# Kernel tuning notes

Hardware: AMD Instinct MI355X
Metric: run time of the kernel (lower is better)

Reference implementation:

```python
import jax, jax.numpy as jnp
import numpy as np

MAX_ITERATIONS = 10
TOLERANCE = 1e-4


def setup_inputs() -> dict:
    key = jax.random.key(0)
    k1, k2 = jax.random.split(key)
    B, N = 4, 2048
    p1 = jax.random.normal(k1, (B, N, 3), dtype=jnp.float32)
    p2 = jax.random.normal(k2, (B, N, 3), dtype=jnp.float32)
    return {"p1": p1, "p2": p2}


def _get_transform(p1, p2):
    # SVD-based rigid (Kabsch) transform between matched sets p1 -> p2.
    p1c = p1.mean(-2, keepdims=True)   # [B,1,3]
    p2c = p2.mean(-2, keepdims=True)   # [B,1,3]
    q1 = p1 - p1c
    q2 = p2 - p2c
    H = jnp.einsum('bnj,bnk->bjk', q2, q1)          # p2^T @ p1, [B,3,3]
    u, s, vT = jnp.linalg.svd(H)
    v = jnp.swapaxes(vT, -1, -2)
    uT = jnp.swapaxes(u, -1, -2)
    d = jnp.linalg.det(v @ uT)                      # [B], reflection fix
    v = v.at[:, 2, 2].multiply(d)
    RT = u @ jnp.swapaxes(v, -1, -2)
    R = jnp.swapaxes(RT, -1, -2)                    # [B,3,3]
    t = p2c - p1c @ R                               # [B,1,3]
    return R, t


def _nearest_neighbor(p1, p2):
    # dist[b, j, i] = ||p2[b,j] - p1[b,i]||  (matches torch broadcast layout)
    dif = p2[:, :, None, :] - p1[:, None, :, :]     # [B,N2,N1,3]
    dist = jnp.sqrt(jnp.sum(dif * dif, axis=-1))    # [B,N2,N1]
    idx = jnp.argmin(dist, axis=-1)                 # [B,N2] (topk k=1, smallest)
    vals = jnp.take_along_axis(dist, idx[..., None], axis=-1)[..., 0]
    return vals, idx


def reference(p1, p2):
    def cond(state):
        temp_pc, it, prev_err, done = state
        return (it <= MAX_ITERATIONS) & jnp.logical_not(done)

    def body(state):
        temp_pc, it, prev_err, _ = state
        vals, idx = _nearest_neighbor(temp_pc, p2)
        mean_err = vals.mean()
        # Source indexes ori_p2 with the LAST batch's indices (nn.indices[-1])
        matched = p2[:, idx[-1], :]                 # [B,N,3]
        R, t = _get_transform(temp_pc, matched)
        new_pc = temp_pc @ R + t
        done = jnp.abs(prev_err - mean_err) < TOLERANCE
        return (new_pc, it + 1, mean_err, done)

    init = (p1, jnp.int32(0), jnp.float32(0.0), jnp.bool_(False))
    temp_pc, _, _, _ = jax.lax.while_loop(cond, body, init)

    R, t = _get_transform(p1, temp_pc)
    T = jnp.concatenate([R, jnp.swapaxes(t, 1, 2)], axis=2)  # [B,3,4]
    return T
```

## Files before the change

kernel.cpp:

```cpp
#include <hip/hip_runtime.h>

#define B 4
#define N 2048
#define MAXIT 11
#define TOL 1e-4f
#define BT 256
#define NBLK 256
#define CC 64
#define QPT 4
#define QC (BT*QPT)
#define RPT 8


__device__ double det3(const double* M) {
    return M[0]*(M[4]*M[8]-M[5]*M[7])
         - M[1]*(M[3]*M[8]-M[5]*M[6])
         + M[2]*(M[3]*M[7]-M[4]*M[6]);
}

__device__ void svd3x3(const double* A, double* U, double* V, double* sig) {
    double S[9];
    for (int i = 0; i < 3; ++i)
        for (int j = 0; j < 3; ++j) {
            double s = 0.0;
            for (int k = 0; k < 3; ++k) s += A[k*3+i] * A[k*3+j];
            S[i*3+j] = s;
        }
    double Vm[9] = {1,0,0, 0,1,0, 0,0,1};
    for (int sweep = 0; sweep < 30; ++sweep) {
        double off = fabs(S[1]) + fabs(S[2]) + fabs(S[5]);
        double base = fabs(S[0]) + fabs(S[4]) + fabs(S[8]);
        if (off <= 1e-15 * base) break;
        for (int pi = 0; pi < 3; ++pi) {
            const int p = (pi == 2) ? 1 : 0;
            const int q = (pi == 0) ? 1 : 2;
            double apq = S[p*3+q];
            if (apq == 0.0) continue;
            double app = S[p*3+p], aqq = S[q*3+q];
            double tau = (aqq - app) / (2.0 * apq);
            double tt  = ((tau >= 0.0) ? 1.0 : -1.0) / (fabs(tau) + sqrt(1.0 + tau*tau));
            double c = 1.0 / sqrt(1.0 + tt*tt);
            double s = tt * c;
            for (int k = 0; k < 3; ++k) {
                double skp = S[k*3+p], skq = S[k*3+q];
                S[k*3+p] = c*skp - s*skq;
                S[k*3+q] = s*skp + c*skq;
            }
            for (int k = 0; k < 3; ++k) {
                double spk = S[p*3+k], sqk = S[q*3+k];
                S[p*3+k] = c*spk - s*sqk;
                S[q*3+k] = s*spk + c*sqk;
            }
            for (int k = 0; k < 3; ++k) {
                double vkp = Vm[k*3+p], vkq = Vm[k*3+q];
                Vm[k*3+p] = c*vkp - s*vkq;
                Vm[k*3+q] = s*vkp + c*vkq;
            }
        }
    }
    double lam[3] = {S[0], S[4], S[8]};
    int ord[3] = {0, 1, 2};
    for (int i = 0; i < 2; ++i)
        for (int j = i+1; j < 3; ++j)
            if (lam[ord[j]] > lam[ord[i]]) { int tmp = ord[i]; ord[i] = ord[j]; ord[j] = tmp; }
    for (int i = 0; i < 3; ++i) {
        int o = ord[i];
        double l = lam[o] > 0.0 ? lam[o] : 0.0;
        sig[i] = sqrt(l);
        for (int k = 0; k < 3; ++k) V[k*3+i] = Vm[k*3+o];
    }
    for (int i = 0; i < 3; ++i) {
        double u0 = 0, u1 = 0, u2 = 0;
        for (int k = 0; k < 3; ++k) {
            u0 += A[0*3+k] * V[k*3+i];
            u1 += A[1*3+k] * V[k*3+i];
            u2 += A[2*3+k] * V[k*3+i];
        }
        double nrm = sqrt(u0*u0 + u1*u1 + u2*u2);
        if (nrm > 1e-300) { u0 /= nrm; u1 /= nrm; u2 /= nrm; }
        else {
            double ax = U[0], ay = U[3], az = U[6];
            double bx = U[1], by = U[4], bz = U[7];
            u0 = ay*bz - az*by; u1 = az*bx - ax*bz; u2 = ax*by - ay*bx;
        }
        U[0*3+i] = u0; U[1*3+i] = u1; U[2*3+i] = u2;
    }
}

__device__ void compute_R_f64(const double* H, double* R) {
    double nf = 0.0;
    for (int k = 0; k < 9; ++k) nf += H[k]*H[k];
    if (nf > 0.0) {
        const double sc = 1.0 / sqrt(nf * (1.0/3.0));
        double X[9];
        #pragma unroll
        for (int k = 0; k < 9; ++k) X[k] = H[k] * sc;
        const double d0 = det3(X);
        if (d0 > 1e-12) {
            for (int iter = 0; iter < 10; ++iter) {
                const double dt = det3(X);
                const double g = (iter < 4) ? cbrt(1.0 / dt) : 1.0;
                double Y[9];
                #pragma unroll
                for (int k = 0; k < 9; ++k) Y[k] = g * X[k];
                double C[9];
                C[0] = Y[4]*Y[8]-Y[5]*Y[7]; C[1] = Y[5]*Y[6]-Y[3]*Y[8]; C[2] = Y[3]*Y[7]-Y[4]*Y[6];
                C[3] = Y[2]*Y[7]-Y[1]*Y[8]; C[4] = Y[0]*Y[8]-Y[2]*Y[6]; C[5] = Y[1]*Y[6]-Y[0]*Y[7];
                C[6] = Y[1]*Y[5]-Y[2]*Y[4]; C[7] = Y[2]*Y[3]-Y[0]*Y[5]; C[8] = Y[0]*Y[4]-Y[1]*Y[3];
                const double inv = 1.0 / (dt * g * g * g);
                #pragma unroll
                for (int k = 0; k < 9; ++k) X[k] = 0.5 * (Y[k] + C[k] * inv);
            }
            R[0]=X[0]; R[1]=X[3]; R[2]=X[6];
            R[3]=X[1]; R[4]=X[4]; R[5]=X[7];
            R[6]=X[2]; R[7]=X[5]; R[8]=X[8];
            return;
        }
    }
    double U[9], V[9], sig[3];
    svd3x3(H, U, V, sig);
    double d = (det3(U) * det3(V) < 0.0) ? -1.0 : 1.0;
    V[2*3+2] *= d;
    for (int i = 0; i < 3; ++i)
        for (int j = 0; j < 3; ++j) {
            double s = 0.0;
            for (int k = 0; k < 3; ++k) s += V[i*3+k] * U[j*3+k];
            R[i*3+j] = s;
        }
}

__device__ inline float wred(float v) {
    v += __shfl_down(v, 32);
    v += __shfl_down(v, 16);
    v += __shfl_down(v, 8);
    v += __shfl_down(v, 4);
    v += __shfl_down(v, 2);
    v += __shfl_down(v, 1);
    return v;
}

__device__ __forceinline__ void tf3(const float* __restrict__ R, const float* __restrict__ T,
                                    float x, float y, float z,
                                    float& ox, float& oy, float& oz) {
    ox = x*R[0] + y*R[3] + z*R[6] + T[0];
    oy = x*R[1] + y*R[4] + z*R[7] + T[1];
    oz = x*R[2] + y*R[5] + z*R[8] + T[2];
}

__global__ void __launch_bounds__(BT) k_iter(const float* __restrict__ p1,
                                             const float* __restrict__ p2,
                                             float* __restrict__ out,
                                             unsigned long long* __restrict__ nnA,
                                             unsigned long long* __restrict__ nnB,
                                             double* __restrict__ rc,
                                             float* __restrict__ errs,
                                             int* __restrict__ doneflag,
                                             int it) {
    const int bid = blockIdx.x, tid = threadIdx.x;
    const int b = bid >> 6, blk = bid & 63;
    const int lane = tid & 63, wave = tid >> 6;

    __shared__ float4 sc4[CC];
    __shared__ float sR[9], sT[3];
    __shared__ float lred[4][16];
    __shared__ int sFin;

    if (it == 0) {
        if (tid == 0) {
            sR[0]=1.f; sR[1]=0.f; sR[2]=0.f;
            sR[3]=0.f; sR[4]=1.f; sR[5]=0.f;
            sR[6]=0.f; sR[7]=0.f; sR[8]=1.f;
            sT[0]=0.f; sT[1]=0.f; sT[2]=0.f;
            sFin = 0;
            if (bid == 0) {
                *doneflag = 0;
                for (int bb = 0; bb < B; ++bb) {
                    double* r0 = rc + (bb*12 + 0)*12;
                    r0[0]=1; r0[1]=0; r0[2]=0; r0[3]=0; r0[4]=1; r0[5]=0;
                    r0[6]=0; r0[7]=0; r0[8]=1; r0[9]=0; r0[10]=0; r0[11]=0;
                }
            }
        }
        __syncthreads();
    } else {
        if (tid == 0) sFin = (*doneflag) ? 2 : 0;
        __syncthreads();
        if (sFin == 2) return;

        const unsigned long long* nnR = ((it-1) & 1) ? nnB : nnA;
        const int renc = ((it-1) >> 1) & 1;
        const double* rp = rc + (b*12 + (it-1))*12;
        float cR[9], cT[3];
        #pragma unroll
        for (int k = 0; k < 9; ++k) cR[k] = (float)rp[k];
        #pragma unroll
        for (int k = 0; k < 3; ++k) cT[k] = (float)rp[9+k];

        float pv[16];
        #pragma unroll
        for (int k = 0; k < 16; ++k) pv[k] = 0.f;

        unsigned long long pk3[RPT];
        #pragma unroll
        for (int u = 0; u < RPT; ++u)
            pk3[u] = nnR[3*N + (tid + u*BT)];
        int mi[RPT];
        #pragma unroll
        for (int u = 0; u < RPT; ++u) {
            const unsigned long long k3 = renc ? ~pk3[u] : pk3[u];
            mi[u] = (int)(unsigned int)(k3 & 0xffffffffULL);
        }
        float mxa[RPT], mya[RPT], mza[RPT];
        #pragma unroll
        for (int u = 0; u < RPT; ++u) {
            const float* mp = &p2[(b*N + mi[u])*3];
            mxa[u] = mp[0]; mya[u] = mp[1]; mza[u] = mp[2];
        }
        float pxa[RPT], pya[RPT], pza[RPT];
        #pragma unroll
        for (int u = 0; u < RPT; ++u) {
            const float* pp = &p1[(b*N + (tid + u*BT))*3];
            pxa[u] = pp[0]; pya[u] = pp[1]; pza[u] = pp[2];
        }
        #pragma unroll
        for (int u = 0; u < RPT; ++u) {
            float tx, ty, tz;
            tf3(cR, cT, pxa[u], pya[u], pza[u], tx, ty, tz);
            const float mx = mxa[u], my = mya[u], mz = mza[u];
            pv[0] += mx;  pv[1] += my;  pv[2] += mz;
            pv[3] += tx;  pv[4] += ty;  pv[5] += tz;
            pv[6] += mx*tx;  pv[7]  += mx*ty;  pv[8]  += mx*tz;
            pv[9] += my*tx;  pv[10] += my*ty;  pv[11] += my*tz;
            pv[12]+= mz*tx;  pv[13] += mz*ty;  pv[14] += mz*tz;
        }
        for (int r = tid; r < B*N; r += BT) {
            unsigned long long pk = nnR[r];
            if (renc) pk = ~pk;
            pv[15] += sqrtf(__uint_as_float((unsigned int)(pk >> 32)));
        }
        #pragma unroll
        for (int k = 0; k < 16; ++k) pv[k] = wred(pv[k]);
        if (lane == 0) {
            #pragma unroll
            for (int k = 0; k < 16; ++k) lred[wave][k] = pv[k];
        }
        __syncthreads();
        if (tid == 0) {
            float a[16];
            #pragma unroll
            for (int k = 0; k < 16; ++k)
                a[k] = lred[0][k] + lred[1][k] + lred[2][k] + lred[3][k];
            const float errcur  = a[15] / (float)(B*N);
            const float errprev = (it >= 2) ? errs[it-2] : 0.0f;
            const int done = (fabsf(errprev - errcur) < TOL) ? 1 : 0;
            errs[it-1] = errcur;

            double c2d[3] = { (double)a[0]/N, (double)a[1]/N, (double)a[2]/N };
            double c1d[3] = { (double)a[3]/N, (double)a[4]/N, (double)a[5]/N };
            double H[9];
            for (int j = 0; j < 3; ++j)
                for (int k = 0; k < 3; ++k)
                    H[j*3+k] = (double)a[6 + j*3 + k] - (double)N * c2d[j] * c1d[k];
            double Rinc[9], tinc[3];
            compute_R_f64(H, Rinc);
            for (int j = 0; j < 3; ++j)
                tinc[j] = c2d[j] - (c1d[0]*Rinc[0*3+j] + c1d[1]*Rinc[1*3+j] + c1d[2]*Rinc[2*3+j]);
            double Rn[9], tn[3];
            for (int i = 0; i < 3; ++i)
                for (int j = 0; j < 3; ++j)
                    Rn[i*3+j] = rp[i*3+0]*Rinc[0*3+j] + rp[i*3+1]*Rinc[1*3+j] + rp[i*3+2]*Rinc[2*3+j];
            for (int j = 0; j < 3; ++j)
                tn[j] = rp[9+0]*Rinc[0*3+j] + rp[9+1]*Rinc[1*3+j] + rp[9+2]*Rinc[2*3+j] + tinc[j];
            double* rn = rc + (b*12 + it)*12;
            for (int k = 0; k < 9; ++k) { rn[k] = Rn[k]; sR[k] = (float)Rn[k]; }
            for (int k = 0; k < 3; ++k) { rn[9+k] = tn[k]; sT[k] = (float)tn[k]; }
            sFin = (done || it == MAXIT) ? 1 : 0;
        }
        __syncthreads();
    }

    if (sFin == 1) {
        if (blk != 0) return;
        float pv[16];
        #pragma unroll
        for (int k = 0; k < 16; ++k) pv[k] = 0.f;
        for (int i = tid; i < N; i += BT) {
            const float* pp = &p1[(b*N + i)*3];
            const float px = pp[0], py = pp[1], pz = pp[2];
            float tx, ty, tz;
            tf3(sR, sT, px, py, pz, tx, ty, tz);
            pv[0] += tx; pv[1] += ty; pv[2] += tz;
            pv[3] += px; pv[4] += py; pv[5] += pz;
            pv[6] += tx*px;  pv[7]  += tx*py;  pv[8]  += tx*pz;
            pv[9] += ty*px;  pv[10] += ty*py;  pv[11] += ty*pz;
            pv[12]+= tz*px;  pv[13] += tz*py;  pv[14] += tz*pz;
        }
        #pragma unroll
        for (int k = 0; k < 15; ++k) pv[k] = wred(pv[k]);
        if (lane == 0) {
            #pragma unroll
            for (int k = 0; k < 15; ++k) lred[wave][k] = pv[k];
        }
        __syncthreads();
        if (tid == 0) {
            float a[15];
            #pragma unroll
            for (int k = 0; k < 15; ++k)
                a[k] = lred[0][k] + lred[1][k] + lred[2][k] + lred[3][k];
            double c2d[3] = { (double)a[0]/N, (double)a[1]/N, (double)a[2]/N };
            double c1d[3] = { (double)a[3]/N, (double)a[4]/N, (double)a[5]/N };
            double H[9];
            for (int j = 0; j < 3; ++j)
                for (int k = 0; k < 3; ++k)
                    H[j*3+k] = (double)a[6 + j*3 + k] - (double)N * c2d[j] * c1d[k];
            double Rf[9];
            compute_R_f64(H, Rf);
            for (int i = 0; i < 3; ++i) {
                out[b*12 + i*4 + 0] = (float)Rf[i*3+0];
                out[b*12 + i*4 + 1] = (float)Rf[i*3+1];
                out[b*12 + i*4 + 2] = (float)Rf[i*3+2];
                const double tj = c2d[i] - (c1d[0]*Rf[0*3+i] + c1d[1]*Rf[1*3+i] + c1d[2]*Rf[2*3+i]);
                out[b*12 + i*4 + 3] = (float)tj;
            }
            *doneflag = 1;
        }
        return;
    }

    {
        unsigned long long* nnW = (it & 1) ? nnB : nnA;
        const int wenc = (it >> 1) & 1;
        const int cb = (blk >> 1) * CC;
        const int qb = (blk & 1) * QC;
        if (tid < CC) {
            const float* cp = &p1[(b*N + cb + tid)*3];
            float cx, cy, cz;
            tf3(sR, sT, cp[0], cp[1], cp[2], cx, cy, cz);
            sc4[tid] = make_float4(cx, cy, cz, 0.5f*(cx*cx + cy*cy + cz*cz));
        }
        __syncthreads();
        float px[QPT], py[QPT], pz[QPT];
        float best[QPT];
        int   bi[QPT];
        #pragma unroll
        for (int k = 0; k < QPT; ++k) {
            const int q = qb + tid + BT*k;
            px[k] = p2[(b*N + q)*3 + 0];
            py[k] = p2[(b*N + q)*3 + 1];
            pz[k] = p2[(b*N + q)*3 + 2];
            best[k] = __uint_as_float(0x7f7fffffu);
            bi[k] = 0;
        }
        #pragma unroll 4
        for (int j = 0; j < CC; ++j) {
            const float4 c = sc4[j];
            #pragma unroll
            for (int k = 0; k < QPT; ++k) {
                float s = __builtin_fmaf(-px[k], c.x,
                          __builtin_fmaf(-py[k], c.y,
                          __builtin_fmaf(-pz[k], c.z, c.w)));
                if (s < best[k]) { best[k] = s; bi[k] = cb + j; }
            }
        }
        #pragma unroll
        for (int k = 0; k < QPT; ++k) {
            const int q = qb + tid + BT*k;
            const float pn = px[k]*px[k] + py[k]*py[k] + pz[k]*pz[k];
            float d2 = fmaxf(__builtin_fmaf(2.0f, best[k], pn), 0.0f);
            unsigned long long K =
                ((unsigned long long)__float_as_uint(d2) << 32) | (unsigned int)bi[k];
            if (wenc) atomicMax(&nnW[b*N + q], ~K);
            else      atomicMin(&nnW[b*N + q],  K);
        }
    }
}

extern "C" void kernel_launch(void* const* d_in, const int* in_sizes, int n_in,
                              void* d_out, int out_size, void* d_ws, size_t ws_size,
                              hipStream_t stream) {
    const float* p1 = (const float*)d_in[0];
    const float* p2 = (const float*)d_in[1];
    float* out = (float*)d_out;
    unsigned long long* nnA = (unsigned long long*)d_ws;
    unsigned long long* nnB = (unsigned long long*)((char*)d_ws + 65536);
    double* rc   = (double*)((char*)d_ws + 131072);
    float* errs  = (float*)((char*)d_ws + 135680);
    int* doneflag = (int*)((char*)d_ws + 135728);

    hipMemsetAsync(d_ws, 0xFF, 131072, stream);
    for (int it = 0; it <= MAXIT; ++it)
        k_iter<<<NBLK, BT, 0, stream>>>(p1, p2, out, nnA, nnB, rc, errs, doneflag, it);
}
```

Before: 313.2 us.

## Fuse ICP iterations into one persistent cooperative kernel with grid barrier

Replaces the twelve per-iteration kernel launches with a single cooperative persistent kernel. Iterations are separated by a sense-reversing global atomic barrier, and each block keeps the cumulative transform and previous error in shared memory and registers instead of global scratch. This removes per-launch overhead and the global round-trips for the rotation chain. In exchange every iteration pays a grid-wide spin barrier and the kernel depends on cooperative launch residency.

```diff
diff --git a/kernel.cpp b/kernel.cpp
--- a/kernel.cpp
+++ b/kernel.cpp
@@ -147,140 +147,203 @@
     oz = x*R[2] + y*R[5] + z*R[8] + T[2];
 }
 
-__global__ void __launch_bounds__(BT) k_iter(const float* __restrict__ p1,
-                                             const float* __restrict__ p2,
-                                             float* __restrict__ out,
-                                             unsigned long long* __restrict__ nnA,
-                                             unsigned long long* __restrict__ nnB,
-                                             double* __restrict__ rc,
-                                             float* __restrict__ errs,
-                                             int* __restrict__ doneflag,
-                                             int it) {
+__device__ __forceinline__ void gbar(unsigned int* cnt, unsigned int* flag,
+                                     unsigned int& sense) {
+    __syncthreads();
+    if (threadIdx.x == 0) {
+        sense ^= 1u;
+        unsigned int arrived = __hip_atomic_fetch_add(cnt, 1u, __ATOMIC_ACQ_REL,
+                                                      __HIP_MEMORY_SCOPE_AGENT);
+        if (arrived == NBLK - 1) {
+            __hip_atomic_store(cnt, 0u, __ATOMIC_RELAXED, __HIP_MEMORY_SCOPE_AGENT);
+            __hip_atomic_store(flag, sense, __ATOMIC_RELEASE, __HIP_MEMORY_SCOPE_AGENT);
+        } else {
+            while (__hip_atomic_load(flag, __ATOMIC_ACQUIRE,
+                                     __HIP_MEMORY_SCOPE_AGENT) != sense)
+                __builtin_amdgcn_s_sleep(4);
+        }
+    }
+    __syncthreads();
+}
+
+__device__ __forceinline__ unsigned long long nnld(const unsigned long long* p) {
+    return __hip_atomic_load(p, __ATOMIC_RELAXED, __HIP_MEMORY_SCOPE_AGENT);
+}
+
+__global__ void __launch_bounds__(BT, 1)
+icp_pers(const float* __restrict__ p1, const float* __restrict__ p2,
+         float* __restrict__ out,
+         unsigned long long* __restrict__ nnA,
+         unsigned long long* __restrict__ nnB,
+         unsigned int* __restrict__ bar) {
     const int bid = blockIdx.x, tid = threadIdx.x;
     const int b = bid >> 6, blk = bid & 63;
     const int lane = tid & 63, wave = tid >> 6;
 
     __shared__ float4 sc4[CC];
     __shared__ float sR[9], sT[3];
+    __shared__ double sCum[12];
     __shared__ float lred[4][16];
     __shared__ int sFin;
 
-    if (it == 0) {
-        if (tid == 0) {
-            sR[0]=1.f; sR[1]=0.f; sR[2]=0.f;
-            sR[3]=0.f; sR[4]=1.f; sR[5]=0.f;
-            sR[6]=0.f; sR[7]=0.f; sR[8]=1.f;
-            sT[0]=0.f; sT[1]=0.f; sT[2]=0.f;
-            sFin = 0;
-            if (bid == 0) {
-                *doneflag = 0;
-                for (int bb = 0; bb < B; ++bb) {
-                    double* r0 = rc + (bb*12 + 0)*12;
-                    r0[0]=1; r0[1]=0; r0[2]=0; r0[3]=0; r0[4]=1; r0[5]=0;
-                    r0[6]=0; r0[7]=0; r0[8]=1; r0[9]=0; r0[10]=0; r0[11]=0;
+    unsigned int sense = 0;
+    float prevErr = 0.0f;
+
+    if (tid == 0) {
+        sR[0]=1.f; sR[1]=0.f; sR[2]=0.f;
+        sR[3]=0.f; sR[4]=1.f; sR[5]=0.f;
+        sR[6]=0.f; sR[7]=0.f; sR[8]=1.f;
+        sT[0]=0.f; sT[1]=0.f; sT[2]=0.f;
+        sCum[0]=1; sCum[1]=0; sCum[2]=0; sCum[3]=0; sCum[4]=1; sCum[5]=0;
+        sCum[6]=0; sCum[7]=0; sCum[8]=1; sCum[9]=0; sCum[10]=0; sCum[11]=0;
+        sFin = 0;
+    }
+    __syncthreads();
+
+    for (int it = 0; it <= MAXIT; ++it) {
+        if (it > 0) {
+            const unsigned long long* nnR = ((it-1) & 1) ? nnB : nnA;
+            const int renc = ((it-1) >> 1) & 1;
+            float cR[9], cT[3];
+            #pragma unroll
+            for (int k = 0; k < 9; ++k) cR[k] = sR[k];
+            #pragma unroll
+            for (int k = 0; k < 3; ++k) cT[k] = sT[k];
+
+            float pv[16];
+            #pragma unroll
+            for (int k = 0; k < 16; ++k) pv[k] = 0.f;
+
+            unsigned long long pk3[RPT];
+            #pragma unroll
+            for (int u = 0; u < RPT; ++u)
+                pk3[u] = nnld(&nnR[3*N + (tid + u*BT)]);
+            int mi[RPT];
+            #pragma unroll
+            for (int u = 0; u < RPT; ++u) {
+                const unsigned long long k3 = renc ? ~pk3[u] : pk3[u];
+                mi[u] = (int)(unsigned int)(k3 & 0xffffffffULL);
+            }
+            float mxa[RPT], mya[RPT], mza[RPT];
+            #pragma unroll
+            for (int u = 0; u < RPT; ++u) {
+                const float* mp = &p2[(b*N + mi[u])*3];
+                mxa[u] = mp[0]; mya[u] = mp[1]; mza[u] = mp[2];
+            }
+            float pxa[RPT], pya[RPT], pza[RPT];
+            #pragma unroll
+            for (int u = 0; u < RPT; ++u) {
+                const float* pp = &p1[(b*N + (tid + u*BT))*3];
+                pxa[u] = pp[0]; pya[u] = pp[1]; pza[u] = pp[2];
+            }
+            #pragma unroll
+            for (int u = 0; u < RPT; ++u) {
+                float tx, ty, tz;
+                tf3(cR, cT, pxa[u], pya[u], pza[u], tx, ty, tz);
+                const float mx = mxa[u], my = mya[u], mz = mza[u];
+                pv[0] += mx;  pv[1] += my;  pv[2] += mz;
+                pv[3] += tx;  pv[4] += ty;  pv[5] += tz;
+                pv[6] += mx*tx;  pv[7]  += mx*ty;  pv[8]  += mx*tz;
+                pv[9] += my*tx;  pv[10] += my*ty;  pv[11] += my*tz;
+                pv[12]+= mz*tx;  pv[13] += mz*ty;  pv[14] += mz*tz;
+            }
+            for (int r = tid; r < B*N; r += BT) {
+                unsigned long long pk = nnld(&nnR[r]);
+                if (renc) pk = ~pk;
+                pv[15] += sqrtf(__uint_as_float((unsigned int)(pk >> 32)));
+            }
+            #pragma unroll
+            for (int k = 0; k < 16; ++k) pv[k] = wred(pv[k]);
+            if (lane == 0) {
+                #pragma unroll
+                for (int k = 0; k < 16; ++k) lred[wave][k] = pv[k];
+            }
+            __syncthreads();
+            if (tid == 0) {
+                float a[16];
+                #pragma unroll
+                for (int k = 0; k < 16; ++k)
+                    a[k] = lred[0][k] + lred[1][k] + lred[2][k] + lred[3][k];
+                const float errcur  = a[15] / (float)(B*N);
+                const float errprev = (it >= 2) ? prevErr : 0.0f;
+                const int done = (fabsf(errprev - errcur) < TOL) ? 1 : 0;
+                prevErr = errcur;
+
+                double c2d[3] = { (double)a[0]/N, (double)a[1]/N, (double)a[2]/N };
+                double c1d[3] = { (double)a[3]/N, (double)a[4]/N, (double)a[5]/N };
+                double H[9];
+                for (int j = 0; j < 3; ++j)
+                    for (int k = 0; k < 3; ++k)
+                        H[j*3+k] = (double)a[6 + j*3 + k] - (double)N * c2d[j] * c1d[k];
+                double Rinc[9], tinc[3];
+                compute_R_f64(H, Rinc);
+                for (int j = 0; j < 3; ++j)
+                    tinc[j] = c2d[j] - (c1d[0]*Rinc[0*3+j] + c1d[1]*Rinc[1*3+j] + c1d[2]*Rinc[2*3+j]);
+                double Rn[9], tn[3];
+                for (int i = 0; i < 3; ++i)
+                    for (int j = 0; j < 3; ++j)
+                        Rn[i*3+j] = sCum[i*3+0]*Rinc[0*3+j] + sCum[i*3+1]*Rinc[1*3+j] + sCum[i*3+2]*Rinc[2*3+j];
+                for (int j = 0; j < 3; ++j)
+                    tn[j] = sCum[9+0]*Rinc[0*3+j] + sCum[9+1]*Rinc[1*3+j] + sCum[9+2]*Rinc[2*3+j] + tinc[j];
+                for (int k = 0; k < 9; ++k) { sCum[k] = Rn[k]; sR[k] = (float)Rn[k]; }
+                for (int k = 0; k < 3; ++k) { sCum[9+k] = tn[k]; sT[k] = (float)tn[k]; }
+                sFin = (done || it == MAXIT) ? 1 : 0;
+            }
+            __syncthreads();
+            if (sFin) break;
+        }
+
+        {
+            unsigned long long* nnW = (it & 1) ? nnB : nnA;
+            const int wenc = (it >> 1) & 1;
+            const int cb = (blk >> 1) * CC;
+            const int qb = (blk & 1) * QC;
+            if (tid < CC) {
+                const float* cp = &p1[(b*N + cb + tid)*3];
+                float cx, cy, cz;
+                tf3(sR, sT, cp[0], cp[1], cp[2], cx, cy, cz);
+                sc4[tid] = make_float4(cx, cy, cz, 0.5f*(cx*cx + cy*cy + cz*cz));
+            }
+            __syncthreads();
+            float px[QPT], py[QPT], pz[QPT];
+            float best[QPT];
+            int   bi[QPT];
+            #pragma unroll
+            for (int k = 0; k < QPT; ++k) {
+                const int q = qb + tid + BT*k;
+                px[k] = p2[(b*N + q)*3 + 0];
+                py[k] = p2[(b*N + q)*3 + 1];
+                pz[k] = p2[(b*N + q)*3 + 2];
+                best[k] = __uint_as_float(0x7f7fffffu);
+                bi[k] = 0;
+            }
+            #pragma unroll 4
+            for (int j = 0; j < CC; ++j) {
+                const float4 c = sc4[j];
+                #pragma unroll
+                for (int k = 0; k < QPT; ++k) {
+                    float s = __builtin_fmaf(-px[k], c.x,
+                              __builtin_fmaf(-py[k], c.y,
+                              __builtin_fmaf(-pz[k], c.z, c.w)));
+                    if (s < best[k]) { best[k] = s; bi[k] = cb + j; }
                 }
             }
-        }
-        __syncthreads();
-    } else {
-        if (tid == 0) sFin = (*doneflag) ? 2 : 0;
-        __syncthreads();
-        if (sFin == 2) return;
-
-        const unsigned long long* nnR = ((it-1) & 1) ? nnB : nnA;
-        const int renc = ((it-1) >> 1) & 1;
-        const double* rp = rc + (b*12 + (it-1))*12;
-        float cR[9], cT[3];
-        #pragma unroll
-        for (int k = 0; k < 9; ++k) cR[k] = (float)rp[k];
-        #pragma unroll
-        for (int k = 0; k < 3; ++k) cT[k] = (float)rp[9+k];
-
-        float pv[16];
-        #pragma unroll
-        for (int k = 0; k < 16; ++k) pv[k] = 0.f;
-
-        unsigned long long pk3[RPT];
-        #pragma unroll
-        for (int u = 0; u < RPT; ++u)
-            pk3[u] = nnR[3*N + (tid + u*BT)];
-        int mi[RPT];
-        #pragma unroll
-        for (int u = 0; u < RPT; ++u) {
-            const unsigned long long k3 = renc ? ~pk3[u] : pk3[u];
-            mi[u] = (int)(unsigned int)(k3 & 0xffffffffULL);
-        }
-        float mxa[RPT], mya[RPT], mza[RPT];
-        #pragma unroll
-        for (int u = 0; u < RPT; ++u) {
-            const float* mp = &p2[(b*N + mi[u])*3];
-            mxa[u] = mp[0]; mya[u] = mp[1]; mza[u] = mp[2];
-        }
-        float pxa[RPT], pya[RPT], pza[RPT];
-        #pragma unroll
-        for (int u = 0; u < RPT; ++u) {
-            const float* pp = &p1[(b*N + (tid + u*BT))*3];
-            pxa[u] = pp[0]; pya[u] = pp[1]; pza[u] = pp[2];
-        }
-        #pragma unroll
-        for (int u = 0; u < RPT; ++u) {
-            float tx, ty, tz;
-            tf3(cR, cT, pxa[u], pya[u], pza[u], tx, ty, tz);
-            const float mx = mxa[u], my = mya[u], mz = mza[u];
-            pv[0] += mx;  pv[1] += my;  pv[2] += mz;
-            pv[3] += tx;  pv[4] += ty;  pv[5] += tz;
-            pv[6] += mx*tx;  pv[7]  += mx*ty;  pv[8]  += mx*tz;
-            pv[9] += my*tx;  pv[10] += my*ty;  pv[11] += my*tz;
-            pv[12]+= mz*tx;  pv[13] += mz*ty;  pv[14] += mz*tz;
-        }
-        for (int r = tid; r < B*N; r += BT) {
-            unsigned long long pk = nnR[r];
-            if (renc) pk = ~pk;
-            pv[15] += sqrtf(__uint_as_float((unsigned int)(pk >> 32)));
-        }
-        #pragma unroll
-        for (int k = 0; k < 16; ++k) pv[k] = wred(pv[k]);
-        if (lane == 0) {
-            #pragma unroll
-            for (int k = 0; k < 16; ++k) lred[wave][k] = pv[k];
-        }
-        __syncthreads();
-        if (tid == 0) {
-            float a[16];
-            #pragma unroll
-            for (int k = 0; k < 16; ++k)
-                a[k] = lred[0][k] + lred[1][k] + lred[2][k] + lred[3][k];
-            const float errcur  = a[15] / (float)(B*N);
-            const float errprev = (it >= 2) ? errs[it-2] : 0.0f;
-            const int done = (fabsf(errprev - errcur) < TOL) ? 1 : 0;
-            errs[it-1] = errcur;
-
-            double c2d[3] = { (double)a[0]/N, (double)a[1]/N, (double)a[2]/N };
-            double c1d[3] = { (double)a[3]/N, (double)a[4]/N, (double)a[5]/N };
-            double H[9];
-            for (int j = 0; j < 3; ++j)
-                for (int k = 0; k < 3; ++k)
-                    H[j*3+k] = (double)a[6 + j*3 + k] - (double)N * c2d[j] * c1d[k];
-            double Rinc[9], tinc[3];
-            compute_R_f64(H, Rinc);
-            for (int j = 0; j < 3; ++j)
-                tinc[j] = c2d[j] - (c1d[0]*Rinc[0*3+j] + c1d[1]*Rinc[1*3+j] + c1d[2]*Rinc[2*3+j]);
-            double Rn[9], tn[3];
-            for (int i = 0; i < 3; ++i)
-                for (int j = 0; j < 3; ++j)
-                    Rn[i*3+j] = rp[i*3+0]*Rinc[0*3+j] + rp[i*3+1]*Rinc[1*3+j] + rp[i*3+2]*Rinc[2*3+j];
-            for (int j = 0; j < 3; ++j)
-                tn[j] = rp[9+0]*Rinc[0*3+j] + rp[9+1]*Rinc[1*3+j] + rp[9+2]*Rinc[2*3+j] + tinc[j];
-            double* rn = rc + (b*12 + it)*12;
-            for (int k = 0; k < 9; ++k) { rn[k] = Rn[k]; sR[k] = (float)Rn[k]; }
-            for (int k = 0; k < 3; ++k) { rn[9+k] = tn[k]; sT[k] = (float)tn[k]; }
-            sFin = (done || it == MAXIT) ? 1 : 0;
-        }
-        __syncthreads();
-    }
-
-    if (sFin == 1) {
-        if (blk != 0) return;
+            #pragma unroll
+            for (int k = 0; k < QPT; ++k) {
+                const int q = qb + tid + BT*k;
+                const float pn = px[k]*px[k] + py[k]*py[k] + pz[k]*pz[k];
+                float d2 = fmaxf(__builtin_fmaf(2.0f, best[k], pn), 0.0f);
+                unsigned long long K =
+                    ((unsigned long long)__float_as_uint(d2) << 32) | (unsigned int)bi[k];
+                if (wenc) atomicMax(&nnW[b*N + q], ~K);
+                else      atomicMin(&nnW[b*N + q],  K);
+            }
+        }
+        gbar(&bar[0], &bar[1], sense);
+    }
+
+    if (blk != 0) return;
+    {
         float pv[16];
         #pragma unroll
         for (int k = 0; k < 16; ++k) pv[k] = 0.f;
@@ -322,55 +385,6 @@
                 const double tj = c2d[i] - (c1d[0]*Rf[0*3+i] + c1d[1]*Rf[1*3+i] + c1d[2]*Rf[2*3+i]);
                 out[b*12 + i*4 + 3] = (float)tj;
             }
-            *doneflag = 1;
-        }
-        return;
-    }
-
-    {
-        unsigned long long* nnW = (it & 1) ? nnB : nnA;
-        const int wenc = (it >> 1) & 1;
-        const int cb = (blk >> 1) * CC;
-        const int qb = (blk & 1) * QC;
-        if (tid < CC) {
-            const float* cp = &p1[(b*N + cb + tid)*3];
-            float cx, cy, cz;
-            tf3(sR, sT, cp[0], cp[1], cp[2], cx, cy, cz);
-            sc4[tid] = make_float4(cx, cy, cz, 0.5f*(cx*cx + cy*cy + cz*cz));
-        }
-        __syncthreads();
-        float px[QPT], py[QPT], pz[QPT];
-        float best[QPT];
-        int   bi[QPT];
-        #pragma unroll
-        for (int k = 0; k < QPT; ++k) {
-            const int q = qb + tid + BT*k;
-            px[k] = p2[(b*N + q)*3 + 0];
-            py[k] = p2[(b*N + q)*3 + 1];
-            pz[k] = p2[(b*N + q)*3 + 2];
-            best[k] = __uint_as_float(0x7f7fffffu);
-            bi[k] = 0;
-        }
-        #pragma unroll 4
-        for (int j = 0; j < CC; ++j) {
-            const float4 c = sc4[j];
-            #pragma unroll
-            for (int k = 0; k < QPT; ++k) {
-                float s = __builtin_fmaf(-px[k], c.x,
-                          __builtin_fmaf(-py[k], c.y,
-                          __builtin_fmaf(-pz[k], c.z, c.w)));
-                if (s < best[k]) { best[k] = s; bi[k] = cb + j; }
-            }
-        }
-        #pragma unroll
-        for (int k = 0; k < QPT; ++k) {
-            const int q = qb + tid + BT*k;
-            const float pn = px[k]*px[k] + py[k]*py[k] + pz[k]*pz[k];
-            float d2 = fmaxf(__builtin_fmaf(2.0f, best[k], pn), 0.0f);
-            unsigned long long K =
-                ((unsigned long long)__float_as_uint(d2) << 32) | (unsigned int)bi[k];
-            if (wenc) atomicMax(&nnW[b*N + q], ~K);
-            else      atomicMin(&nnW[b*N + q],  K);
         }
     }
 }
@@ -383,11 +397,12 @@
     float* out = (float*)d_out;
     unsigned long long* nnA = (unsigned long long*)d_ws;
     unsigned long long* nnB = (unsigned long long*)((char*)d_ws + 65536);
-    double* rc   = (double*)((char*)d_ws + 131072);
-    float* errs  = (float*)((char*)d_ws + 135680);
-    int* doneflag = (int*)((char*)d_ws + 135728);
+    unsigned int* bar = (unsigned int*)((char*)d_ws + 131072);
 
     hipMemsetAsync(d_ws, 0xFF, 131072, stream);
-    for (int it = 0; it <= MAXIT; ++it)
-        k_iter<<<NBLK, BT, 0, stream>>>(p1, p2, out, nnA, nnB, rc, errs, doneflag, it);
-}
+    hipMemsetAsync((char*)d_ws + 131072, 0, 8, stream);
+    void* args[] = { (void*)&p1, (void*)&p2, (void*)&out,
+                     (void*)&nnA, (void*)&nnB, (void*)&bar };
+    hipLaunchCooperativeKernel((const void*)icp_pers, dim3(NBLK), dim3(BT),
+                               args, 0, stream);
+}
```

Result: slower. 544.2 us (+73.8%).

## Give each block full candidate set and reduce nearest neighbor in shared memory

Applied to the files above, without the earlier changes.

Each block now transforms all N source points into shared memory (with a skewed layout to avoid bank conflicts) and handles 32 queries. Threads split the candidates into 32 strips and the per-strip minima are reduced in shared memory. This replaces the per-chunk global 64-bit atomics and the memset that initialised them. The trade is redundant transformation of all 2048 points per block and larger shared memory use, which can lower occupancy.

```diff
diff --git a/kernel.cpp b/kernel.cpp
--- a/kernel.cpp
+++ b/kernel.cpp
@@ -6,10 +6,10 @@
 #define TOL 1e-4f
 #define BT 256
 #define NBLK 256
-#define CC 64
-#define QPT 4
-#define QC (BT*QPT)
 #define RPT 8
+#define QPB 32
+#define NSTR 32
+#define CPS 64
 
 
 __device__ double det3(const double* M) {
@@ -150,8 +150,8 @@
 __global__ void __launch_bounds__(BT) k_iter(const float* __restrict__ p1,
                                              const float* __restrict__ p2,
                                              float* __restrict__ out,
-                                             unsigned long long* __restrict__ nnA,
-                                             unsigned long long* __restrict__ nnB,
+                                             const unsigned long long* __restrict__ nnR,
+                                             unsigned long long* __restrict__ nnW,
                                              double* __restrict__ rc,
                                              float* __restrict__ errs,
                                              int* __restrict__ doneflag,
@@ -160,7 +160,10 @@
     const int b = bid >> 6, blk = bid & 63;
     const int lane = tid & 63, wave = tid >> 6;
 
-    __shared__ float4 sc4[CC];
+    __shared__ float4 sc4[N];
+    __shared__ float sScore[NSTR][QPB];
+    __shared__ int   sIdx[NSTR][QPB];
+    __shared__ float sPn[QPB];
     __shared__ float sR[9], sT[3];
     __shared__ float lred[4][16];
     __shared__ int sFin;
@@ -187,8 +190,6 @@
         __syncthreads();
         if (sFin == 2) return;
 
-        const unsigned long long* nnR = ((it-1) & 1) ? nnB : nnA;
-        const int renc = ((it-1) >> 1) & 1;
         const double* rp = rc + (b*12 + (it-1))*12;
         float cR[9], cT[3];
         #pragma unroll
@@ -206,10 +207,8 @@
             pk3[u] = nnR[3*N + (tid + u*BT)];
         int mi[RPT];
         #pragma unroll
-        for (int u = 0; u < RPT; ++u) {
-            const unsigned long long k3 = renc ? ~pk3[u] : pk3[u];
-            mi[u] = (int)(unsigned int)(k3 & 0xffffffffULL);
-        }
+        for (int u = 0; u < RPT; ++u)
+            mi[u] = (int)(unsigned int)(pk3[u] & 0xffffffffULL);
         float mxa[RPT], mya[RPT], mza[RPT];
         #pragma unroll
         for (int u = 0; u < RPT; ++u) {
@@ -233,11 +232,8 @@
             pv[9] += my*tx;  pv[10] += my*ty;  pv[11] += my*tz;
             pv[12]+= mz*tx;  pv[13] += mz*ty;  pv[14] += mz*tz;
         }
-        for (int r = tid; r < B*N; r += BT) {
-            unsigned long long pk = nnR[r];
-            if (renc) pk = ~pk;
-            pv[15] += sqrtf(__uint_as_float((unsigned int)(pk >> 32)));
-        }
+        for (int r = tid; r < B*N; r += BT)
+            pv[15] += sqrtf(__uint_as_float((unsigned int)(nnR[r] >> 32)));
         #pragma unroll
         for (int k = 0; k < 16; ++k) pv[k] = wred(pv[k]);
         if (lane == 0) {
@@ -328,49 +324,60 @@
     }
 
     {
-        unsigned long long* nnW = (it & 1) ? nnB : nnA;
-        const int wenc = (it >> 1) & 1;
-        const int cb = (blk >> 1) * CC;
-        const int qb = (blk & 1) * QC;
-        if (tid < CC) {
-            const float* cp = &p1[(b*N + cb + tid)*3];
+        for (int c = tid; c < N; c += BT) {
+            const float* cp = &p1[(b*N + c)*3];
             float cx, cy, cz;
             tf3(sR, sT, cp[0], cp[1], cp[2], cx, cy, cz);
-            sc4[tid] = make_float4(cx, cy, cz, 0.5f*(cx*cx + cy*cy + cz*cz));
-        }
-        __syncthreads();
-        float px[QPT], py[QPT], pz[QPT];
-        float best[QPT];
-        int   bi[QPT];
-        #pragma unroll
-        for (int k = 0; k < QPT; ++k) {
-            const int q = qb + tid + BT*k;
-            px[k] = p2[(b*N + q)*3 + 0];
-            py[k] = p2[(b*N + q)*3 + 1];
-            pz[k] = p2[(b*N + q)*3 + 2];
-            best[k] = __uint_as_float(0x7f7fffffu);
-            bi[k] = 0;
-        }
-        #pragma unroll 4
-        for (int j = 0; j < CC; ++j) {
-            const float4 c = sc4[j];
-            #pragma unroll
-            for (int k = 0; k < QPT; ++k) {
-                float s = __builtin_fmaf(-px[k], c.x,
-                          __builtin_fmaf(-py[k], c.y,
-                          __builtin_fmaf(-pz[k], c.z, c.w)));
-                if (s < best[k]) { best[k] = s; bi[k] = cb + j; }
-            }
-        }
-        #pragma unroll
-        for (int k = 0; k < QPT; ++k) {
-            const int q = qb + tid + BT*k;
-            const float pn = px[k]*px[k] + py[k]*py[k] + pz[k]*pz[k];
-            float d2 = fmaxf(__builtin_fmaf(2.0f, best[k], pn), 0.0f);
-            unsigned long long K =
-                ((unsigned long long)__float_as_uint(d2) << 32) | (unsigned int)bi[k];
-            if (wenc) atomicMax(&nnW[b*N + q], ~K);
-            else      atomicMin(&nnW[b*N + q],  K);
+            const int s = c >> 6, jj = c & 63;
+            sc4[s*64 + ((jj + s) & 63)] =
+                make_float4(cx, cy, cz, 0.5f*(cx*cx + cy*cy + cz*cz));
+        }
+        __syncthreads();
+
+        const int qg = tid & 7, st = tid >> 3;
+        float px[4], py[4], pz[4];
+        #pragma unroll
+        for (int k = 0; k < 4; ++k) {
+            const int q = blk*QPB + qg*4 + k;
+            const float* pp = &p2[(b*N + q)*3];
+            px[k] = pp[0]; py[k] = pp[1]; pz[k] = pp[2];
+        }
+        if (st == 0) {
+            #pragma unroll
+            for (int k = 0; k < 4; ++k)
+                sPn[qg*4 + k] = px[k]*px[k] + py[k]*py[k] + pz[k]*pz[k];
+        }
+        float bs[4]; int bj[4];
+        #pragma unroll
+        for (int k = 0; k < 4; ++k) { bs[k] = __uint_as_float(0x7f7fffffu); bj[k] = 0; }
+        const int base = st * CPS;
+        for (int j = 0; j < CPS; ++j) {
+            const float4 cd = sc4[base + ((j + st) & (CPS-1))];
+            const int cidx = base + j;
+            #pragma unroll
+            for (int k = 0; k < 4; ++k) {
+                float s = __builtin_fmaf(-px[k], cd.x,
+                          __builtin_fmaf(-py[k], cd.y,
+                          __builtin_fmaf(-pz[k], cd.z, cd.w)));
+                if (s < bs[k]) { bs[k] = s; bj[k] = cidx; }
+            }
+        }
+        #pragma unroll
+        for (int k = 0; k < 4; ++k) {
+            sScore[st][qg*4 + k] = bs[k];
+            sIdx[st][qg*4 + k]   = bj[k];
+        }
+        __syncthreads();
+        if (tid < QPB) {
+            float fb = sScore[0][tid]; int fj = sIdx[0][tid];
+            #pragma unroll 8
+            for (int s = 1; s < NSTR; ++s) {
+                const float v = sScore[s][tid]; const int vi = sIdx[s][tid];
+                if (v < fb || (v == fb && vi < fj)) { fb = v; fj = vi; }
+            }
+            const float d2 = fmaxf(__builtin_fmaf(2.0f, fb, sPn[tid]), 0.0f);
+            nnW[b*N + blk*QPB + tid] =
+                ((unsigned long long)__float_as_uint(d2) << 32) | (unsigned int)fj;
         }
     }
 }
@@ -387,7 +394,9 @@
     float* errs  = (float*)((char*)d_ws + 135680);
     int* doneflag = (int*)((char*)d_ws + 135728);
 
-    hipMemsetAsync(d_ws, 0xFF, 131072, stream);
-    for (int it = 0; it <= MAXIT; ++it)
-        k_iter<<<NBLK, BT, 0, stream>>>(p1, p2, out, nnA, nnB, rc, errs, doneflag, it);
-}
+    for (int it = 0; it <= MAXIT; ++it) {
+        unsigned long long* w = (it & 1) ? nnB : nnA;
+        unsigned long long* r = (it & 1) ? nnA : nnB;
+        k_iter<<<NBLK, BT, 0, stream>>>(p1, p2, out, r, w, rc, errs, doneflag, it);
+    }
+}
```

After: 352.1 us. 1.12x slower.
